# Performance work log

Hardware: AMD Instinct MI355X
Metric: run time of the kernel (lower is better)

The kernel has to match this reference:

```python
import jax, jax.numpy as jnp
import numpy as np

TEMPERATURE = 0.1
EPS = 1e-08
NEG_INF = -9e15


def setup_inputs() -> dict:
    key = jax.random.key(0)
    k1, k2 = jax.random.split(key)
    B, D = 4096, 256
    z_i = jax.random.normal(k1, (B, D), dtype=jnp.float32)
    z_j = jax.random.normal(k2, (B, D), dtype=jnp.float32)
    mask_positive = jnp.ones((B,), dtype=bool)
    return {"z_i": z_i, "z_j": z_j, "mask_positive": mask_positive}


def reference(z_i, z_j, mask_positive):
    B = z_i.shape[0]
    N = 2 * B
    z = jnp.concatenate([z_i, z_j], axis=0)  # [N, D]
    # cosine similarity: normalize (norms clamped to eps) then GEMM
    norms = jnp.maximum(jnp.linalg.norm(z, axis=1, keepdims=True), EPS)
    zn = z / norms
    sim = jnp.matmul(zn, zn.T) / TEMPERATURE  # [N, N]
    # mask self-similarity on diagonal
    rows = jnp.arange(N)
    sim = sim.at[rows, rows].set(NEG_INF)
    logprob = jax.nn.log_softmax(sim, axis=1)
    # positive of row k is row (k+B) mod N
    positives = jnp.concatenate([jnp.arange(B, N), jnp.arange(0, B)])
    loss_vec = -logprob[rows, positives]  # [N]
    mp = jnp.concatenate([mask_positive, mask_positive])  # [N] bool
    cnt = jnp.sum(mp.astype(jnp.float32))
    total = jnp.sum(jnp.where(mp, loss_vec, 0.0))
    loss = jnp.where(cnt > 0, total / jnp.maximum(cnt, 1.0), 0.0)
    return loss
```

## Files before the change

### kernel.cpp

```cpp
#include <hip/hip_runtime.h>
#include <hip/hip_bf16.h>

#define NTOT   8192
#define BHALF  4096
#define DDIM   256
#define TEMP_INV 10.0f
#define BM     128
#define BN     64
#define CSPLIT 8
#define LDSTRIDE 280

typedef __attribute__((ext_vector_type(8))) short bf16x8_t;
typedef __attribute__((ext_vector_type(4))) float f32x4_t;

__device__ inline unsigned short f2bf(float x) {
    __hip_bfloat16 h = __float2bfloat16(x);
    return __builtin_bit_cast(unsigned short, h);
}
__device__ inline float bf2f(unsigned short u) {
    return __bfloat162float(__builtin_bit_cast(__hip_bfloat16, u));
}

__global__ void norm_cast_kernel(const float* __restrict__ zi,
                                 const float* __restrict__ zj,
                                 unsigned short* __restrict__ zn) {
    int gtid = blockIdx.x * blockDim.x + threadIdx.x;
    int row  = gtid >> 6;
    int lane = gtid & 63;
    const float* src = (row < BHALF) ? (zi + (size_t)row * DDIM)
                                     : (zj + (size_t)(row - BHALF) * DDIM);
    float4 v = reinterpret_cast<const float4*>(src)[lane];
    float ss = v.x*v.x + v.y*v.y + v.z*v.z + v.w*v.w;
    #pragma unroll
    for (int off = 32; off >= 1; off >>= 1) ss += __shfl_xor(ss, off);
    float scale = 1.0f / fmaxf(sqrtf(ss), 1e-8f);
    ushort4 o;
    o.x = f2bf(v.x * scale);
    o.y = f2bf(v.y * scale);
    o.z = f2bf(v.z * scale);
    o.w = f2bf(v.w * scale);
    reinterpret_cast<ushort4*>(zn + (size_t)row * DDIM)[lane] = o;
}

__global__ void posdot_kernel(const unsigned short* __restrict__ zn,
                              float* __restrict__ posdot) {
    int gtid = blockIdx.x * blockDim.x + threadIdx.x;
    int k    = gtid >> 6;
    int lane = gtid & 63;
    ushort4 ua = reinterpret_cast<const ushort4*>(zn + (size_t)k * DDIM)[lane];
    ushort4 ub = reinterpret_cast<const ushort4*>(zn + (size_t)(k + BHALF) * DDIM)[lane];
    float s = bf2f(ua.x)*bf2f(ub.x) + bf2f(ua.y)*bf2f(ub.y)
            + bf2f(ua.z)*bf2f(ub.z) + bf2f(ua.w)*bf2f(ub.w);
    #pragma unroll
    for (int off = 32; off >= 1; off >>= 1) s += __shfl_xor(s, off);
    if (lane == 0) posdot[k] = s * TEMP_INV;
}

__global__ void __launch_bounds__(256)
gemm_expsum_kernel(const unsigned short* __restrict__ zn,
                   float* __restrict__ s_arr) {
    __shared__ unsigned short ldsB[64 * LDSTRIDE];
    const int tid  = threadIdx.x;
    const int lane = tid & 63;
    const int wv   = tid >> 6;
    const int m    = lane & 15;
    const int quad = lane >> 4;
    const int R0   = blockIdx.x * BM;
    const int CB   = blockIdx.y * (NTOT / CSPLIT);

    bf16x8_t afrag[2][8];
    #pragma unroll
    for (int rf = 0; rf < 2; ++rf) {
        const unsigned short* arow = zn + (size_t)(R0 + wv*32 + rf*16 + m) * DDIM;
        #pragma unroll
        for (int kk = 0; kk < 8; ++kk)
            afrag[rf][kk] = *reinterpret_cast<const bf16x8_t*>(arow + kk*32 + quad*8);
    }

    float expacc[2][4] = {{0.f,0.f,0.f,0.f},{0.f,0.f,0.f,0.f}};

    for (int it = 0; it < (NTOT / CSPLIT) / BN; ++it) {
        const int C0 = CB + it * BN;
        __syncthreads();
        #pragma unroll
        for (int s = 0; s < 8; ++s) {
            int ci = s * 256 + tid;
            int n = ci >> 5, c = ci & 31;
            bf16x8_t v = *reinterpret_cast<const bf16x8_t*>(zn + (size_t)(C0 + n) * DDIM + c * 8);
            *reinterpret_cast<bf16x8_t*>(&ldsB[n * LDSTRIDE + c * 8]) = v;
        }
        __syncthreads();

        f32x4_t cacc[2][4];
        #pragma unroll
        for (int rf = 0; rf < 2; ++rf)
            #pragma unroll
            for (int cf = 0; cf < 4; ++cf)
                cacc[rf][cf] = (f32x4_t){0.f, 0.f, 0.f, 0.f};

        #pragma unroll
        for (int kk = 0; kk < 8; ++kk) {
            bf16x8_t b[4];
            #pragma unroll
            for (int cf = 0; cf < 4; ++cf)
                b[cf] = *reinterpret_cast<const bf16x8_t*>(
                            &ldsB[(cf*16 + m) * LDSTRIDE + kk*32 + quad*8]);
            #pragma unroll
            for (int cf = 0; cf < 4; ++cf)
                #pragma unroll
                for (int rf = 0; rf < 2; ++rf)
                    cacc[rf][cf] = __builtin_amdgcn_mfma_f32_16x16x32_bf16(
                        afrag[rf][kk], b[cf], cacc[rf][cf], 0, 0, 0);
        }

        #pragma unroll
        for (int rf = 0; rf < 2; ++rf) {
            #pragma unroll
            for (int cf = 0; cf < 4; ++cf) {
                int gc = C0 + cf*16 + m;
                #pragma unroll
                for (int r = 0; r < 4; ++r) {
                    int gr = R0 + wv*32 + rf*16 + quad*4 + r;
                    float e = __expf(cacc[rf][cf][r] * TEMP_INV);
                    expacc[rf][r] += (gr == gc) ? 0.0f : e;
                }
            }
        }
    }

    #pragma unroll
    for (int rf = 0; rf < 2; ++rf)
        #pragma unroll
        for (int r = 0; r < 4; ++r) {
            float v = expacc[rf][r];
            v += __shfl_xor(v, 1);
            v += __shfl_xor(v, 2);
            v += __shfl_xor(v, 4);
            v += __shfl_xor(v, 8);
            if (m == 0)
                atomicAdd(&s_arr[R0 + wv*32 + rf*16 + quad*4 + r], v);
        }
}

__global__ void finalize_kernel(const float* __restrict__ s_arr,
                                const float* __restrict__ posdot,
                                const unsigned char* __restrict__ mask,
                                float* __restrict__ out) {
    int tid = threadIdx.x, lane = tid & 63, wv = tid >> 6;
    float tot = 0.f, cnt = 0.f;
    for (int k = tid; k < NTOT; k += 256) {
        int kb = k & (BHALF - 1);
        if (mask[kb] != 0) {
            tot += logf(s_arr[k]) - posdot[kb];
            cnt += 1.f;
        }
    }
    #pragma unroll
    for (int off = 32; off >= 1; off >>= 1) {
        tot += __shfl_xor(tot, off);
        cnt += __shfl_xor(cnt, off);
    }
    __shared__ float st[4], sc[4];
    if (lane == 0) { st[wv] = tot; sc[wv] = cnt; }
    __syncthreads();
    if (tid == 0) {
        float T = st[0] + st[1] + st[2] + st[3];
        float C = sc[0] + sc[1] + sc[2] + sc[3];
        out[0] = (C > 0.f) ? (T / fmaxf(C, 1.f)) : 0.f;
    }
}

extern "C" void kernel_launch(void* const* d_in, const int* in_sizes, int n_in,
                              void* d_out, int out_size, void* d_ws, size_t ws_size,
                              hipStream_t stream) {
    const float* zi = (const float*)d_in[0];
    const float* zj = (const float*)d_in[1];
    const unsigned char* mask = (const unsigned char*)d_in[2];
    float* out = (float*)d_out;

    unsigned short* zn = (unsigned short*)d_ws;
    float* s_arr  = (float*)((char*)d_ws + (size_t)NTOT * DDIM * 2);
    float* posdot = s_arr + NTOT;

    hipMemsetAsync(s_arr, 0, NTOT * sizeof(float), stream);
    norm_cast_kernel<<<dim3(NTOT / 4), dim3(256), 0, stream>>>(zi, zj, zn);
    posdot_kernel<<<dim3(BHALF / 4), dim3(256), 0, stream>>>(zn, posdot);
    gemm_expsum_kernel<<<dim3(NTOT / BM, CSPLIT), dim3(256), 0, stream>>>(zn, s_arr);
    finalize_kernel<<<dim3(1), dim3(256), 0, stream>>>(s_arr, posdot, mask, out);
}
```

Measured before the change: 129.8 us.

## Exploit similarity-matrix symmetry to halve GEMM work and fuse normalization with positive dot

The GEMM now covers only upper-triangular tiles (256-row by 64-column blocks). Each exp value is added both to its row sum and, through column atomics, to its column sum, so roughly half the MFMA and exp work is skipped. The normalize, positive-dot and memset steps are merged into one kernel that computes the positive dot in fp32 from the raw inputs. The finalize kernel runs with 1024 threads and uses the fast log. This adds many more atomics, a serial tile-index decode loop and heavier register pressure from 4x8 A fragments. Positive dots are no longer taken from the bf16-rounded values, which slightly shifts numerics.

```diff
diff --git a/kernel.cpp b/kernel.cpp
--- a/kernel.cpp
+++ b/kernel.cpp
@@ -5,10 +5,8 @@
 #define BHALF  4096
 #define DDIM   256
 #define TEMP_INV 10.0f
-#define BM     128
 #define BN     64
-#define CSPLIT 8
-#define LDSTRIDE 280
+#define LDSTRIDE 264
 
 typedef __attribute__((ext_vector_type(8))) short bf16x8_t;
 typedef __attribute__((ext_vector_type(4))) float f32x4_t;
@@ -17,128 +15,126 @@
     __hip_bfloat16 h = __float2bfloat16(x);
     return __builtin_bit_cast(unsigned short, h);
 }
-__device__ inline float bf2f(unsigned short u) {
-    return __bfloat162float(__builtin_bit_cast(__hip_bfloat16, u));
+
+__global__ void norm_pair_kernel(const float* __restrict__ zi,
+                                 const float* __restrict__ zj,
+                                 unsigned short* __restrict__ zn,
+                                 float* __restrict__ posdot,
+                                 float* __restrict__ s_arr) {
+    int gtid = blockIdx.x * 256 + threadIdx.x;
+    if (gtid < NTOT) s_arr[gtid] = 0.0f;
+    int k    = gtid >> 6;
+    int lane = gtid & 63;
+    float4 vi = reinterpret_cast<const float4*>(zi + (size_t)k * DDIM)[lane];
+    float4 vj = reinterpret_cast<const float4*>(zj + (size_t)k * DDIM)[lane];
+    float ssi = vi.x*vi.x + vi.y*vi.y + vi.z*vi.z + vi.w*vi.w;
+    float ssj = vj.x*vj.x + vj.y*vj.y + vj.z*vj.z + vj.w*vj.w;
+    float dot = vi.x*vj.x + vi.y*vj.y + vi.z*vj.z + vi.w*vj.w;
+    #pragma unroll
+    for (int off = 32; off >= 1; off >>= 1) {
+        ssi += __shfl_xor(ssi, off);
+        ssj += __shfl_xor(ssj, off);
+        dot += __shfl_xor(dot, off);
+    }
+    float ri = 1.0f / fmaxf(sqrtf(ssi), 1e-8f);
+    float rj = 1.0f / fmaxf(sqrtf(ssj), 1e-8f);
+    ushort4 oi, oj;
+    oi.x = f2bf(vi.x * ri); oi.y = f2bf(vi.y * ri);
+    oi.z = f2bf(vi.z * ri); oi.w = f2bf(vi.w * ri);
+    oj.x = f2bf(vj.x * rj); oj.y = f2bf(vj.y * rj);
+    oj.z = f2bf(vj.z * rj); oj.w = f2bf(vj.w * rj);
+    reinterpret_cast<ushort4*>(zn + (size_t)k * DDIM)[lane] = oi;
+    reinterpret_cast<ushort4*>(zn + (size_t)(k + BHALF) * DDIM)[lane] = oj;
+    if (lane == 0) posdot[k] = dot * ri * rj * TEMP_INV;
 }
 
-__global__ void norm_cast_kernel(const float* __restrict__ zi,
-                                 const float* __restrict__ zj,
-                                 unsigned short* __restrict__ zn) {
-    int gtid = blockIdx.x * blockDim.x + threadIdx.x;
-    int row  = gtid >> 6;
-    int lane = gtid & 63;
-    const float* src = (row < BHALF) ? (zi + (size_t)row * DDIM)
-                                     : (zj + (size_t)(row - BHALF) * DDIM);
-    float4 v = reinterpret_cast<const float4*>(src)[lane];
-    float ss = v.x*v.x + v.y*v.y + v.z*v.z + v.w*v.w;
-    #pragma unroll
-    for (int off = 32; off >= 1; off >>= 1) ss += __shfl_xor(ss, off);
-    float scale = 1.0f / fmaxf(sqrtf(ss), 1e-8f);
-    ushort4 o;
-    o.x = f2bf(v.x * scale);
-    o.y = f2bf(v.y * scale);
-    o.z = f2bf(v.z * scale);
-    o.w = f2bf(v.w * scale);
-    reinterpret_cast<ushort4*>(zn + (size_t)row * DDIM)[lane] = o;
-}
+__global__ void __launch_bounds__(256, 2)
+gemm_sym_kernel(const unsigned short* __restrict__ zn,
+                float* __restrict__ s_arr) {
+    __shared__ unsigned short ldsB[BN * LDSTRIDE];
 
-__global__ void posdot_kernel(const unsigned short* __restrict__ zn,
-                              float* __restrict__ posdot) {
-    int gtid = blockIdx.x * blockDim.x + threadIdx.x;
-    int k    = gtid >> 6;
-    int lane = gtid & 63;
-    ushort4 ua = reinterpret_cast<const ushort4*>(zn + (size_t)k * DDIM)[lane];
-    ushort4 ub = reinterpret_cast<const ushort4*>(zn + (size_t)(k + BHALF) * DDIM)[lane];
-    float s = bf2f(ua.x)*bf2f(ub.x) + bf2f(ua.y)*bf2f(ub.y)
-            + bf2f(ua.z)*bf2f(ub.z) + bf2f(ua.w)*bf2f(ub.w);
-    #pragma unroll
-    for (int off = 32; off >= 1; off >>= 1) s += __shfl_xor(s, off);
-    if (lane == 0) posdot[k] = s * TEMP_INV;
-}
+    int id = blockIdx.x;
+    int bi = 0;
+    while (id >= 128 - 4 * bi) { id -= 128 - 4 * bi; ++bi; }
+    const int cs = 4 * bi + id;
+    const int R0 = bi << 8;
+    const int C0 = cs << 6;
+    const bool isDiag = ((cs >> 2) == bi);
 
-__global__ void __launch_bounds__(256)
-gemm_expsum_kernel(const unsigned short* __restrict__ zn,
-                   float* __restrict__ s_arr) {
-    __shared__ unsigned short ldsB[64 * LDSTRIDE];
     const int tid  = threadIdx.x;
     const int lane = tid & 63;
     const int wv   = tid >> 6;
     const int m    = lane & 15;
     const int quad = lane >> 4;
-    const int R0   = blockIdx.x * BM;
-    const int CB   = blockIdx.y * (NTOT / CSPLIT);
 
-    bf16x8_t afrag[2][8];
+    bf16x8_t afrag[4][8];
     #pragma unroll
-    for (int rf = 0; rf < 2; ++rf) {
-        const unsigned short* arow = zn + (size_t)(R0 + wv*32 + rf*16 + m) * DDIM;
+    for (int rf = 0; rf < 4; ++rf) {
+        const unsigned short* arow = zn + (size_t)(R0 + wv*64 + rf*16 + m) * DDIM;
         #pragma unroll
         for (int kk = 0; kk < 8; ++kk)
             afrag[rf][kk] = *reinterpret_cast<const bf16x8_t*>(arow + kk*32 + quad*8);
     }
 
-    float expacc[2][4] = {{0.f,0.f,0.f,0.f},{0.f,0.f,0.f,0.f}};
+    #pragma unroll
+    for (int s = 0; s < 8; ++s) {
+        int ci = s * 256 + tid;
+        int n = ci >> 5, c = ci & 31;
+        bf16x8_t v = *reinterpret_cast<const bf16x8_t*>(zn + (size_t)(C0 + n) * DDIM + c * 8);
+        *reinterpret_cast<bf16x8_t*>(&ldsB[n * LDSTRIDE + c * 8]) = v;
+    }
+    __syncthreads();
 
-    for (int it = 0; it < (NTOT / CSPLIT) / BN; ++it) {
-        const int C0 = CB + it * BN;
-        __syncthreads();
+    float rowacc[4][4] = {{0.f,0.f,0.f,0.f},{0.f,0.f,0.f,0.f},
+                          {0.f,0.f,0.f,0.f},{0.f,0.f,0.f,0.f}};
+
+    #pragma unroll
+    for (int cf = 0; cf < 4; ++cf) {
+        f32x4_t cacc[4];
         #pragma unroll
-        for (int s = 0; s < 8; ++s) {
-            int ci = s * 256 + tid;
-            int n = ci >> 5, c = ci & 31;
-            bf16x8_t v = *reinterpret_cast<const bf16x8_t*>(zn + (size_t)(C0 + n) * DDIM + c * 8);
-            *reinterpret_cast<bf16x8_t*>(&ldsB[n * LDSTRIDE + c * 8]) = v;
-        }
-        __syncthreads();
-
-        f32x4_t cacc[2][4];
-        #pragma unroll
-        for (int rf = 0; rf < 2; ++rf)
-            #pragma unroll
-            for (int cf = 0; cf < 4; ++cf)
-                cacc[rf][cf] = (f32x4_t){0.f, 0.f, 0.f, 0.f};
+        for (int rf = 0; rf < 4; ++rf) cacc[rf] = (f32x4_t){0.f,0.f,0.f,0.f};
 
         #pragma unroll
         for (int kk = 0; kk < 8; ++kk) {
-            bf16x8_t b[4];
+            bf16x8_t b = *reinterpret_cast<const bf16x8_t*>(
+                             &ldsB[(cf*16 + m) * LDSTRIDE + kk*32 + quad*8]);
             #pragma unroll
-            for (int cf = 0; cf < 4; ++cf)
-                b[cf] = *reinterpret_cast<const bf16x8_t*>(
-                            &ldsB[(cf*16 + m) * LDSTRIDE + kk*32 + quad*8]);
-            #pragma unroll
-            for (int cf = 0; cf < 4; ++cf)
-                #pragma unroll
-                for (int rf = 0; rf < 2; ++rf)
-                    cacc[rf][cf] = __builtin_amdgcn_mfma_f32_16x16x32_bf16(
-                        afrag[rf][kk], b[cf], cacc[rf][cf], 0, 0, 0);
+            for (int rf = 0; rf < 4; ++rf)
+                cacc[rf] = __builtin_amdgcn_mfma_f32_16x16x32_bf16(
+                    afrag[rf][kk], b, cacc[rf], 0, 0, 0);
         }
 
+        const int gc = C0 + cf*16 + m;
+        float colsum = 0.f;
         #pragma unroll
-        for (int rf = 0; rf < 2; ++rf) {
+        for (int rf = 0; rf < 4; ++rf) {
             #pragma unroll
-            for (int cf = 0; cf < 4; ++cf) {
-                int gc = C0 + cf*16 + m;
-                #pragma unroll
-                for (int r = 0; r < 4; ++r) {
-                    int gr = R0 + wv*32 + rf*16 + quad*4 + r;
-                    float e = __expf(cacc[rf][cf][r] * TEMP_INV);
-                    expacc[rf][r] += (gr == gc) ? 0.0f : e;
-                }
+            for (int r = 0; r < 4; ++r) {
+                int gr = R0 + wv*64 + rf*16 + quad*4 + r;
+                float e = __expf(cacc[rf][r] * TEMP_INV);
+                if (isDiag && gr == gc) e = 0.f;
+                rowacc[rf][r] += e;
+                colsum += e;
             }
+        }
+        if (!isDiag) {
+            colsum += __shfl_xor(colsum, 16);
+            colsum += __shfl_xor(colsum, 32);
+            if (quad == 0) atomicAdd(&s_arr[gc], colsum);
         }
     }
 
     #pragma unroll
-    for (int rf = 0; rf < 2; ++rf)
+    for (int rf = 0; rf < 4; ++rf)
         #pragma unroll
         for (int r = 0; r < 4; ++r) {
-            float v = expacc[rf][r];
+            float v = rowacc[rf][r];
             v += __shfl_xor(v, 1);
             v += __shfl_xor(v, 2);
             v += __shfl_xor(v, 4);
             v += __shfl_xor(v, 8);
             if (m == 0)
-                atomicAdd(&s_arr[R0 + wv*32 + rf*16 + quad*4 + r], v);
+                atomicAdd(&s_arr[R0 + wv*64 + rf*16 + quad*4 + r], v);
         }
 }
 
@@ -148,10 +144,12 @@
                                 float* __restrict__ out) {
     int tid = threadIdx.x, lane = tid & 63, wv = tid >> 6;
     float tot = 0.f, cnt = 0.f;
-    for (int k = tid; k < NTOT; k += 256) {
+    #pragma unroll
+    for (int s = 0; s < NTOT / 1024; ++s) {
+        int k = s * 1024 + tid;
         int kb = k & (BHALF - 1);
         if (mask[kb] != 0) {
-            tot += logf(s_arr[k]) - posdot[kb];
+            tot += __logf(s_arr[k]) - posdot[kb];
             cnt += 1.f;
         }
     }
@@ -160,12 +158,13 @@
         tot += __shfl_xor(tot, off);
         cnt += __shfl_xor(cnt, off);
     }
-    __shared__ float st[4], sc[4];
+    __shared__ float st[16], sc[16];
     if (lane == 0) { st[wv] = tot; sc[wv] = cnt; }
     __syncthreads();
     if (tid == 0) {
-        float T = st[0] + st[1] + st[2] + st[3];
-        float C = sc[0] + sc[1] + sc[2] + sc[3];
+        float T = 0.f, C = 0.f;
+        #pragma unroll
+        for (int i = 0; i < 16; ++i) { T += st[i]; C += sc[i]; }
         out[0] = (C > 0.f) ? (T / fmaxf(C, 1.f)) : 0.f;
     }
 }
@@ -182,9 +181,7 @@
     float* s_arr  = (float*)((char*)d_ws + (size_t)NTOT * DDIM * 2);
     float* posdot = s_arr + NTOT;
 
-    hipMemsetAsync(s_arr, 0, NTOT * sizeof(float), stream);
-    norm_cast_kernel<<<dim3(NTOT / 4), dim3(256), 0, stream>>>(zi, zj, zn);
-    posdot_kernel<<<dim3(BHALF / 4), dim3(256), 0, stream>>>(zn, posdot);
-    gemm_expsum_kernel<<<dim3(NTOT / BM, CSPLIT), dim3(256), 0, stream>>>(zn, s_arr);
-    finalize_kernel<<<dim3(1), dim3(256), 0, stream>>>(s_arr, posdot, mask, out);
+    norm_pair_kernel<<<dim3(1024), dim3(256), 0, stream>>>(zi, zj, zn, posdot, s_arr);
+    gemm_sym_kernel<<<dim3(2112), dim3(256), 0, stream>>>(zn, s_arr);
+    finalize_kernel<<<dim3(1), dim3(1024), 0, stream>>>(s_arr, posdot, mask, out);
 }
```

Measured after the change: 134.4 us. 1.04x slower.
